# Kernel optimization log

Hardware: AMD Instinct MI355X
Metric: run time of the kernel (lower is better)

## Reference

```python
import jax, jax.numpy as jnp
import numpy as np

H = 16       # num_heads
DH = 64      # dim_head
SCALE = DH ** -0.5


def setup_inputs() -> dict:
    key = jax.random.key(0)
    k1, k2 = jax.random.split(key)
    ZT = jax.random.normal(k1, (2, 2048, 1024), dtype=jnp.float32)
    # Linear weight, shape (H*dh, dim); scaled like a typical init for stability
    W = jax.random.normal(k2, (1024, 1024), dtype=jnp.float32) * 0.02
    return {"ZT": ZT, "W": W}


def reference(ZT, W):
    b, n, dim = ZT.shape
    # UT(ZT): ZT @ W^T -> (b, n, H*dh), reshape to (b, h, n, dh)
    ZTU = jnp.einsum('bnd,ed->bne', ZT, W).reshape(b, n, H, DH).transpose(0, 2, 1, 3)
    # scores = ZTU @ ZTU^T * scale  (b, h, n, n)
    scores = jnp.einsum('bhnd,bhmd->bhnm', ZTU, ZTU) * SCALE
    attn = jax.nn.softmax(scores, axis=-1)  # dropout p=0 -> identity
    # attn @ ZTU -> (b, h, n, dh) -> (b, n, H*dh)
    ssa = jnp.einsum('bhnm,bhmd->bhnd', attn, ZTU)
    ssa = ssa.transpose(0, 2, 1, 3).reshape(b, n, H * DH)
    # UT(I).T == W (shape (H*dh, dim)); final projection back to dim
    mssa = jnp.einsum('bne,ed->bnd', ssa, W)
    # return_proj=False path: module returns (MSSA_out, MSSA_out)
    return (mssa, mssa)
```

## Files before the change

### kernel.cpp

```cpp
#include <hip/hip_runtime.h>
#include <hip/hip_bf16.h>
#include <stdint.h>

typedef __attribute__((ext_vector_type(8))) short bf16x8;
typedef __attribute__((ext_vector_type(4))) float f32x4;

#define MFMA16(a, b, c) __builtin_amdgcn_mfma_f32_16x16x32_bf16(a, b, c, 0, 0, 0)

typedef const __attribute__((address_space(1))) unsigned int* as1_u32p;
typedef __attribute__((address_space(3))) unsigned int* as3_u32p;
__device__ __forceinline__ void gl_lds16(const void* g, void* l) {
    __builtin_amdgcn_global_load_lds((as1_u32p)g, (as3_u32p)l, 16, 0, 0);
}

__device__ __forceinline__ unsigned short f2bs(float f) {
    __hip_bfloat16 h = __float2bfloat16(f);
    unsigned short s;
    __builtin_memcpy(&s, &h, 2);
    return s;
}

__device__ __forceinline__ unsigned int pk_bf16(float a, float b) {
    float2 f; f.x = a; f.y = b;
    __hip_bfloat162 h = __float22bfloat162_rn(f);
    unsigned int u;
    __builtin_memcpy(&u, &h, 4);
    return u;
}

__device__ __forceinline__ float exp2_raw(float x) {
    float r;
    asm("v_exp_f32 %0, %1" : "=v"(r) : "v"(x));
    return r;
}

#define QSCALE 0.18033688f

__global__ __launch_bounds__(256) void cvt_w_k(const float* __restrict__ w,
                                               unsigned short* __restrict__ wbf,
                                               unsigned short* __restrict__ wtbf) {
    __shared__ __attribute__((aligned(16))) unsigned short T[64 * 72];
    const int b2 = blockIdx.x;
    const int tid = threadIdx.x;
    const int e0 = (b2 >> 4) * 64, d0 = (b2 & 15) * 64;
    const int el = tid >> 2;
    const int dl = (tid & 3) * 16;
    const float* src = w + (size_t)(e0 + el) * 1024 + d0 + dl;
    unsigned short myv[16];
#pragma unroll
    for (int q = 0; q < 4; ++q) {
        const float4 v = *(const float4*)(src + q * 4);
        myv[q * 4 + 0] = f2bs(v.x);
        myv[q * 4 + 1] = f2bs(v.y);
        myv[q * 4 + 2] = f2bs(v.z);
        myv[q * 4 + 3] = f2bs(v.w);
    }
    *(bf16x8*)(wbf + (size_t)(e0 + el) * 1024 + d0 + dl) = *(const bf16x8*)&myv[0];
    *(bf16x8*)(wbf + (size_t)(e0 + el) * 1024 + d0 + dl + 8) = *(const bf16x8*)&myv[8];
    const int epl = 4 * (el & 15) + (el >> 4);
#pragma unroll
    for (int q = 0; q < 16; ++q) T[(dl + q) * 72 + epl] = myv[q];
    __syncthreads();
#pragma unroll
    for (int p = 0; p < 2; ++p) {
        const int idx = p * 256 + tid;
        const int dd = idx >> 3, c = (idx & 7) * 8;
        const bf16x8 v = *(const bf16x8*)&T[dd * 72 + c];
        *(bf16x8*)(wtbf + (size_t)(d0 + dd) * 1024 + e0 + c) = v;
    }
}

template <int EPI>
__global__ __launch_bounds__(256, 2) void gemm_bt_k(
    const float* __restrict__ Af32, const __hip_bfloat16* __restrict__ Abf,
    const __hip_bfloat16* __restrict__ B,
    unsigned short* __restrict__ ztu, unsigned short* __restrict__ ztut,
    float* __restrict__ out0, float* __restrict__ out1) {
    __shared__ __attribute__((aligned(16))) unsigned short smem[12288];
    unsigned short* At = smem;
    unsigned short* Bt = smem + 4096;
    unsigned short* Tb = smem;

    const int p = blockIdx.x;
    const int bm = (p & 7) * 8 + ((p >> 3) & 7);
    const int bn = p >> 6;
    const int tid = threadIdx.x;
    const int wave = tid >> 6, lane = tid & 63;
    const int wm = wave >> 1, wn = wave & 1;
    const int quad = lane >> 4, l16 = lane & 15;

    f32x4 acc[2][4] = {};

    const int lr = lane >> 2, lc = (lane & 3) * 8;
    const float* Agf = Af32 ? Af32 + (size_t)(bm * 64 + wave * 16 + lr) * 1024 + lc : nullptr;
    const __hip_bfloat16* Agb =
        Abf ? Abf + (size_t)(bm * 64 + wave * 16 + lr) * 1024 + lc : nullptr;
    const __hip_bfloat16* Bg0 = B + (size_t)(bn * 128 + (2 * wave) * 16 + lr) * 1024 + lc;
    const __hip_bfloat16* Bg1 = B + (size_t)(bn * 128 + (2 * wave + 1) * 16 + lr) * 1024 + lc;
    unsigned short* lA = At + wave * 512;
    unsigned short* lB0 = Bt + (2 * wave) * 512;
    unsigned short* lB1 = Bt + (2 * wave + 1) * 512;

    for (int kt = 0; kt < 16; ++kt) {
        const int ko = kt << 6;
        if (EPI == 0) {
#pragma unroll
            for (int h = 0; h < 2; ++h) {
                const float4 v0 = *(const float4*)(Agf + ko + h * 32);
                const float4 v1 = *(const float4*)(Agf + ko + h * 32 + 4);
                uint4 wv;
                wv.x = pk_bf16(v0.x, v0.y);
                wv.y = pk_bf16(v0.z, v0.w);
                wv.z = pk_bf16(v1.x, v1.y);
                wv.w = pk_bf16(v1.z, v1.w);
                *(uint4*)(lA + h * 2048 + lr * 32 + lc) = wv;
            }
        } else {
            gl_lds16(Agb + ko, lA);
            gl_lds16(Agb + ko + 32, lA + 2048);
        }
        gl_lds16(Bg0 + ko, lB0);
        gl_lds16(Bg0 + ko + 32, lB0 + 4096);
        gl_lds16(Bg1 + ko, lB1);
        gl_lds16(Bg1 + ko + 32, lB1 + 4096);
        __syncthreads();
        bf16x8 af[2][2], bfr[2][4];
#pragma unroll
        for (int h = 0; h < 2; ++h)
#pragma unroll
            for (int i = 0; i < 2; ++i)
                af[h][i] = *(const bf16x8*)&At[h * 2048 + (wm * 32 + i * 16 + l16) * 32 + quad * 8];
#pragma unroll
        for (int h = 0; h < 2; ++h)
#pragma unroll
            for (int j = 0; j < 4; ++j)
                bfr[h][j] = *(const bf16x8*)&Bt[h * 4096 + (wn * 64 + j * 16 + l16) * 32 + quad * 8];
#pragma unroll
        for (int h = 0; h < 2; ++h)
#pragma unroll
            for (int i = 0; i < 2; ++i)
#pragma unroll
                for (int j = 0; j < 4; ++j) acc[i][j] = MFMA16(af[h][i], bfr[h][j], acc[i][j]);
        __syncthreads();
    }

    if (EPI == 0) {
        const int h = bn * 2 + wn;
        const int bb = bm >> 5;
        const int nb = (bm & 31) * 64;
        const size_t hb = (size_t)(bb * 16 + h) * 131072;
#pragma unroll
        for (int i = 0; i < 2; ++i) {
#pragma unroll
            for (int r = 0; r < 4; ++r) {
                const int n = nb + wm * 32 + i * 16 + quad * 4 + r;
                uint2 pk;
                pk.x = pk_bf16(acc[i][0][r], acc[i][1][r]);
                pk.y = pk_bf16(acc[i][2][r], acc[i][3][r]);
                *(uint2*)(ztu + hb + n * 64 + l16 * 4) = pk;
                const int npl = 16 * quad + 4 * r + 2 * wm + i;
                Tb[(wn * 64 + 0 + l16) * 72 + npl] = (unsigned short)(pk.x & 0xffff);
                Tb[(wn * 64 + 16 + l16) * 72 + npl] = (unsigned short)(pk.x >> 16);
                Tb[(wn * 64 + 32 + l16) * 72 + npl] = (unsigned short)(pk.y & 0xffff);
                Tb[(wn * 64 + 48 + l16) * 72 + npl] = (unsigned short)(pk.y >> 16);
            }
        }
        __syncthreads();
#pragma unroll
        for (int ee = 0; ee < 4; ++ee) {
            const int e_local = wave * 32 + ee * 8 + (lane >> 3);
            const int nc = (lane & 7) * 8;
            const bf16x8 v = *(const bf16x8*)&Tb[e_local * 72 + nc];
            const int hh = bn * 2 + (e_local >> 6);
            const int dh = e_local & 63;
            *(bf16x8*)(ztut + (size_t)(bb * 16 + hh) * 131072 + dh * 2048 + nb + nc) = v;
        }
    } else {
#pragma unroll
        for (int i = 0; i < 2; ++i) {
#pragma unroll
            for (int r = 0; r < 4; ++r) {
                const int mm = bm * 64 + wm * 32 + i * 16 + quad * 4 + r;
#pragma unroll
                for (int j = 0; j < 4; ++j) {
                    const int e = bn * 128 + wn * 64 + j * 16 + l16;
                    const float v = acc[i][j][r];
                    out0[(size_t)mm * 1024 + e] = v;
                    out1[(size_t)mm * 1024 + e] = v;
                }
            }
        }
    }
}

__global__ __launch_bounds__(256, 4) void attn_k(const unsigned short* __restrict__ ztu,
                                                 const unsigned short* __restrict__ ztut,
                                                 unsigned short* __restrict__ ssa) {
    __shared__ __attribute__((aligned(16))) unsigned short Kt[64 * 64];
    __shared__ __attribute__((aligned(16))) unsigned short Vt[64 * 64];
    __shared__ __attribute__((aligned(16))) unsigned short Pt[4][32 * 72];
    const int p = blockIdx.x;
    const int ii = p >> 3;
    const int bh = (p & 7) * 4 + (ii >> 4);
    const int qt = ii & 15;
    const int tid = threadIdx.x, wave = tid >> 6, lane = tid & 63;
    const int quad = lane >> 4, l16 = lane & 15;
    const unsigned short* base = ztu + (size_t)bh * 131072;
    const unsigned short* baseT = ztut + (size_t)bh * 131072;

    const int qb = qt * 128 + wave * 32;
    bf16x8 qa[2][2];
#pragma unroll
    for (int g = 0; g < 2; ++g) {
        qa[g][0] = *(const bf16x8*)(base + (qb + g * 16 + l16) * 64 + quad * 8);
        qa[g][1] = *(const bf16x8*)(base + (qb + g * 16 + l16) * 64 + 32 + quad * 8);
    }

    float lsum[2][4] = {};
    f32x4 o[2][4] = {};

    const int c0 = wave * 2, c1 = c0 + 1;
    const int lrow = lane >> 3;
    const int sw = (lane & 7) ^ lrow;
    const unsigned short* gK0 = base + (c0 * 8 + lrow) * 64 + sw * 8;
    const unsigned short* gK1 = base + (c1 * 8 + lrow) * 64 + sw * 8;
    const unsigned short* gV0 = baseT + (size_t)(c0 * 8 + lrow) * 2048 + sw * 8;
    const unsigned short* gV1 = baseT + (size_t)(c1 * 8 + lrow) * 2048 + sw * 8;
    unsigned short* lK0 = &Kt[c0 * 512];
    unsigned short* lK1 = &Kt[c1 * 512];
    unsigned short* lV0 = &Vt[c0 * 512];
    unsigned short* lV1 = &Vt[c1 * 512];
    unsigned short* pw = &Pt[wave][0];

    const int swq = (quad ^ (l16 & 7));
    const int koff0 = l16 * 64 + swq * 8;
    const int koff1 = l16 * 64 + (swq ^ 4) * 8;

    for (int t = 0; t < 32; ++t) {
        gl_lds16(gK0 + t * 4096, lK0);
        gl_lds16(gK1 + t * 4096, lK1);
        gl_lds16(gV0 + t * 64, lV0);
        gl_lds16(gV1 + t * 64, lV1);
        __syncthreads();

        f32x4 s[2][4];
#pragma unroll
        for (int nf = 0; nf < 4; ++nf) {
            bf16x8 kb0 = *(const bf16x8*)&Kt[nf * 1024 + koff0];
            bf16x8 kb1 = *(const bf16x8*)&Kt[nf * 1024 + koff1];
#pragma unroll
            for (int g = 0; g < 2; ++g) {
                f32x4 z = {0.f, 0.f, 0.f, 0.f};
                z = MFMA16(qa[g][0], kb0, z);
                z = MFMA16(qa[g][1], kb1, z);
                s[g][nf] = z;
            }
        }

#pragma unroll
        for (int g = 0; g < 2; ++g) {
#pragma unroll
            for (int r = 0; r < 4; ++r) {
                const float p0 = exp2_raw(s[g][0][r] * QSCALE);
                const float p1 = exp2_raw(s[g][1][r] * QSCALE);
                const float p2 = exp2_raw(s[g][2][r] * QSCALE);
                const float p3 = exp2_raw(s[g][3][r] * QSCALE);
                lsum[g][r] += (p0 + p1) + (p2 + p3);
                uint2 pk;
                pk.x = pk_bf16(p0, p1);
                pk.y = pk_bf16(p2, p3);
                *(uint2*)&pw[(g * 16 + quad * 4 + r) * 72 + l16 * 4] = pk;
            }
        }
        asm volatile("s_waitcnt lgkmcnt(0)" ::: "memory");

        bf16x8 pa[2][2];
#pragma unroll
        for (int g = 0; g < 2; ++g) {
            pa[g][0] = *(const bf16x8*)&pw[(g * 16 + l16) * 72 + quad * 8];
            pa[g][1] = *(const bf16x8*)&pw[(g * 16 + l16) * 72 + 32 + quad * 8];
        }
#pragma unroll
        for (int df = 0; df < 4; ++df) {
            bf16x8 vb0 = *(const bf16x8*)&Vt[df * 1024 + koff0];
            bf16x8 vb1 = *(const bf16x8*)&Vt[df * 1024 + koff1];
#pragma unroll
            for (int g = 0; g < 2; ++g) {
                o[g][df] = MFMA16(pa[g][0], vb0, o[g][df]);
                o[g][df] = MFMA16(pa[g][1], vb1, o[g][df]);
            }
        }
        __syncthreads();
    }

    const int b = bh >> 4, h = bh & 15;
#pragma unroll
    for (int g = 0; g < 2; ++g) {
#pragma unroll
        for (int r = 0; r < 4; ++r) {
            float v = lsum[g][r];
            v += __shfl_xor(v, 1);
            v += __shfl_xor(v, 2);
            v += __shfl_xor(v, 4);
            v += __shfl_xor(v, 8);
            const float inv = 1.0f / v;
            const int token = b * 2048 + qt * 128 + wave * 32 + g * 16 + quad * 4 + r;
            uint2 pk;
            pk.x = pk_bf16(o[g][0][r] * inv, o[g][1][r] * inv);
            pk.y = pk_bf16(o[g][2][r] * inv, o[g][3][r] * inv);
            *(uint2*)(ssa + (size_t)token * 1024 + h * 64 + l16 * 4) = pk;
        }
    }
}

extern "C" void kernel_launch(void* const* d_in, const int* in_sizes, int n_in,
                              void* d_out, int out_size, void* d_ws, size_t ws_size,
                              hipStream_t stream) {
    const float* ZT = (const float*)d_in[0];
    const float* W = (const float*)d_in[1];
    float* out = (float*)d_out;
    char* ws = (char*)d_ws;

    unsigned short* wbf   = (unsigned short*)(ws);
    unsigned short* wtbf  = (unsigned short*)(ws + 2u * 1024 * 1024);
    unsigned short* ztu   = (unsigned short*)(ws + 4u * 1024 * 1024);
    unsigned short* ztut  = (unsigned short*)(ws + 12u * 1024 * 1024);
    unsigned short* ssabf = (unsigned short*)(ws + 20u * 1024 * 1024);

    cvt_w_k<<<256, 256, 0, stream>>>(W, wbf, wtbf);
    gemm_bt_k<0><<<512, 256, 0, stream>>>(ZT, nullptr, (const __hip_bfloat16*)wbf, ztu, ztut,
                                          nullptr, nullptr);
    attn_k<<<512, 256, 0, stream>>>(ztu, ztut, ssabf);
    gemm_bt_k<1><<<512, 256, 0, stream>>>(nullptr, (const __hip_bfloat16*)ssabf,
                                          (const __hip_bfloat16*)wtbf, nullptr, nullptr, out,
                                          out + 4194304);
}
```

Baseline: 162.8 us.

## Compute transposed scores so softmax probabilities feed PV MFMA directly from registers

Swaps the MFMA operand order so each lane holds the transposed score tile, letting the exponentiated probabilities be packed straight into the A-operand registers for the PV MFMA instead of round-tripping through a per-wave LDS buffer. This drops the P shared-memory array, its writes and reads, and the lgkmcnt wait. Row sums become per-lane with a cross-quad shuffle, and the output store layout changes to match. The key/column permutations in the transpose/epilogue are adjusted to be consistent, and the attention launch bounds drop from 4 to 2 blocks per SM, which may change occupancy.

```diff
diff --git a/kernel.cpp b/kernel.cpp
--- a/kernel.cpp
+++ b/kernel.cpp
@@ -57,9 +57,8 @@
     }
     *(bf16x8*)(wbf + (size_t)(e0 + el) * 1024 + d0 + dl) = *(const bf16x8*)&myv[0];
     *(bf16x8*)(wbf + (size_t)(e0 + el) * 1024 + d0 + dl + 8) = *(const bf16x8*)&myv[8];
-    const int epl = 4 * (el & 15) + (el >> 4);
-#pragma unroll
-    for (int q = 0; q < 16; ++q) T[(dl + q) * 72 + epl] = myv[q];
+#pragma unroll
+    for (int q = 0; q < 16; ++q) T[(dl + q) * 72 + el] = myv[q];
     __syncthreads();
 #pragma unroll
     for (int p = 0; p < 2; ++p) {
@@ -158,7 +157,7 @@
                 pk.x = pk_bf16(acc[i][0][r], acc[i][1][r]);
                 pk.y = pk_bf16(acc[i][2][r], acc[i][3][r]);
                 *(uint2*)(ztu + hb + n * 64 + l16 * 4) = pk;
-                const int npl = 16 * quad + 4 * r + 2 * wm + i;
+                const int npl = wm * 32 + quad * 8 + i * 4 + r;
                 Tb[(wn * 64 + 0 + l16) * 72 + npl] = (unsigned short)(pk.x & 0xffff);
                 Tb[(wn * 64 + 16 + l16) * 72 + npl] = (unsigned short)(pk.x >> 16);
                 Tb[(wn * 64 + 32 + l16) * 72 + npl] = (unsigned short)(pk.y & 0xffff);
@@ -193,12 +192,11 @@
     }
 }
 
-__global__ __launch_bounds__(256, 4) void attn_k(const unsigned short* __restrict__ ztu,
+__global__ __launch_bounds__(256, 2) void attn_k(const unsigned short* __restrict__ ztu,
                                                  const unsigned short* __restrict__ ztut,
                                                  unsigned short* __restrict__ ssa) {
     __shared__ __attribute__((aligned(16))) unsigned short Kt[64 * 64];
     __shared__ __attribute__((aligned(16))) unsigned short Vt[64 * 64];
-    __shared__ __attribute__((aligned(16))) unsigned short Pt[4][32 * 72];
     const int p = blockIdx.x;
     const int ii = p >> 3;
     const int bh = (p & 7) * 4 + (ii >> 4);
@@ -216,7 +214,7 @@
         qa[g][1] = *(const bf16x8*)(base + (qb + g * 16 + l16) * 64 + 32 + quad * 8);
     }
 
-    float lsum[2][4] = {};
+    float lsum[2] = {0.f, 0.f};
     f32x4 o[2][4] = {};
 
     const int c0 = wave * 2, c1 = c0 + 1;
@@ -230,7 +228,6 @@
     unsigned short* lK1 = &Kt[c1 * 512];
     unsigned short* lV0 = &Vt[c0 * 512];
     unsigned short* lV1 = &Vt[c1 * 512];
-    unsigned short* pw = &Pt[wave][0];
 
     const int swq = (quad ^ (l16 & 7));
     const int koff0 = l16 * 64 + swq * 8;
@@ -243,7 +240,7 @@
         gl_lds16(gV1 + t * 64, lV1);
         __syncthreads();
 
-        f32x4 s[2][4];
+        f32x4 st[2][4];
 #pragma unroll
         for (int nf = 0; nf < 4; ++nf) {
             bf16x8 kb0 = *(const bf16x8*)&Kt[nf * 1024 + koff0];
@@ -251,43 +248,41 @@
 #pragma unroll
             for (int g = 0; g < 2; ++g) {
                 f32x4 z = {0.f, 0.f, 0.f, 0.f};
-                z = MFMA16(qa[g][0], kb0, z);
-                z = MFMA16(qa[g][1], kb1, z);
-                s[g][nf] = z;
-            }
-        }
-
+                z = MFMA16(kb0, qa[g][0], z);
+                z = MFMA16(kb1, qa[g][1], z);
+                st[g][nf] = z;
+            }
+        }
+
+        bf16x8 pa[2][2];
 #pragma unroll
         for (int g = 0; g < 2; ++g) {
-#pragma unroll
-            for (int r = 0; r < 4; ++r) {
-                const float p0 = exp2_raw(s[g][0][r] * QSCALE);
-                const float p1 = exp2_raw(s[g][1][r] * QSCALE);
-                const float p2 = exp2_raw(s[g][2][r] * QSCALE);
-                const float p3 = exp2_raw(s[g][3][r] * QSCALE);
-                lsum[g][r] += (p0 + p1) + (p2 + p3);
-                uint2 pk;
-                pk.x = pk_bf16(p0, p1);
-                pk.y = pk_bf16(p2, p3);
-                *(uint2*)&pw[(g * 16 + quad * 4 + r) * 72 + l16 * 4] = pk;
-            }
-        }
-        asm volatile("s_waitcnt lgkmcnt(0)" ::: "memory");
-
-        bf16x8 pa[2][2];
-#pragma unroll
-        for (int g = 0; g < 2; ++g) {
-            pa[g][0] = *(const bf16x8*)&pw[(g * 16 + l16) * 72 + quad * 8];
-            pa[g][1] = *(const bf16x8*)&pw[(g * 16 + l16) * 72 + 32 + quad * 8];
-        }
+            float e[16];
+#pragma unroll
+            for (int nf = 0; nf < 4; ++nf)
+#pragma unroll
+                for (int r = 0; r < 4; ++r) e[nf * 4 + r] = exp2_raw(st[g][nf][r] * QSCALE);
+            float s0 = 0.f, s1 = 0.f;
+#pragma unroll
+            for (int q = 0; q < 8; ++q) { s0 += e[q]; s1 += e[q + 8]; }
+            lsum[g] += s0 + s1;
+            uint4 u0, u1;
+            u0.x = pk_bf16(e[0], e[1]);   u0.y = pk_bf16(e[2], e[3]);
+            u0.z = pk_bf16(e[4], e[5]);   u0.w = pk_bf16(e[6], e[7]);
+            u1.x = pk_bf16(e[8], e[9]);   u1.y = pk_bf16(e[10], e[11]);
+            u1.z = pk_bf16(e[12], e[13]); u1.w = pk_bf16(e[14], e[15]);
+            __builtin_memcpy(&pa[g][0], &u0, 16);
+            __builtin_memcpy(&pa[g][1], &u1, 16);
+        }
+
 #pragma unroll
         for (int df = 0; df < 4; ++df) {
             bf16x8 vb0 = *(const bf16x8*)&Vt[df * 1024 + koff0];
             bf16x8 vb1 = *(const bf16x8*)&Vt[df * 1024 + koff1];
 #pragma unroll
             for (int g = 0; g < 2; ++g) {
-                o[g][df] = MFMA16(pa[g][0], vb0, o[g][df]);
-                o[g][df] = MFMA16(pa[g][1], vb1, o[g][df]);
+                o[g][df] = MFMA16(vb0, pa[g][0], o[g][df]);
+                o[g][df] = MFMA16(vb1, pa[g][1], o[g][df]);
             }
         }
         __syncthreads();
@@ -296,19 +291,17 @@
     const int b = bh >> 4, h = bh & 15;
 #pragma unroll
     for (int g = 0; g < 2; ++g) {
-#pragma unroll
-        for (int r = 0; r < 4; ++r) {
-            float v = lsum[g][r];
-            v += __shfl_xor(v, 1);
-            v += __shfl_xor(v, 2);
-            v += __shfl_xor(v, 4);
-            v += __shfl_xor(v, 8);
-            const float inv = 1.0f / v;
-            const int token = b * 2048 + qt * 128 + wave * 32 + g * 16 + quad * 4 + r;
+        float v = lsum[g];
+        v += __shfl_xor(v, 16);
+        v += __shfl_xor(v, 32);
+        const float inv = 1.0f / v;
+        const int token = b * 2048 + qb + g * 16 + l16;
+#pragma unroll
+        for (int df = 0; df < 4; ++df) {
             uint2 pk;
-            pk.x = pk_bf16(o[g][0][r] * inv, o[g][1][r] * inv);
-            pk.y = pk_bf16(o[g][2][r] * inv, o[g][3][r] * inv);
-            *(uint2*)(ssa + (size_t)token * 1024 + h * 64 + l16 * 4) = pk;
+            pk.x = pk_bf16(o[g][df][0] * inv, o[g][df][1] * inv);
+            pk.y = pk_bf16(o[g][df][2] * inv, o[g][df][3] * inv);
+            *(uint2*)(ssa + (size_t)token * 1024 + h * 64 + df * 16 + quad * 4) = pk;
         }
     }
 }
```

New measurement: 159.1 us. 1.02x faster.
